# Kernel optimization log

Measured on AMD Instinct MI355X. Metric: run time of the kernel, lower is better.

Reference implementation:

```python
import jax, jax.numpy as jnp
import numpy as np

B, S, D, L = 16, 512, 768, 5
MAX_W, TOP_K = 5, 8


def setup_inputs() -> dict:
    key = jax.random.key(0)
    ks = jax.random.split(key, 6)
    token_embs = jax.random.normal(ks[0], (B, S, D), dtype=jnp.float32)
    token_mask = jnp.ones((B, S), dtype=jnp.int32)
    label_embs = jax.random.normal(ks[1], (B, L, D), dtype=jnp.float32)
    W1 = jax.random.normal(ks[2], (2 * D, D), dtype=jnp.float32) / np.sqrt(2 * D)
    b1 = jnp.zeros((D,), dtype=jnp.float32)
    W2 = jax.random.normal(ks[3], (D, D), dtype=jnp.float32) / np.sqrt(D)
    b2 = jnp.zeros((D,), dtype=jnp.float32)
    Ws = jax.random.normal(ks[4], (D,), dtype=jnp.float32) / np.sqrt(D)
    bs = jnp.zeros((), dtype=jnp.float32)
    return {"token_embs": token_embs, "token_mask": token_mask,
            "label_embs": label_embs, "W1": W1, "b1": b1,
            "W2": W2, "b2": b2, "Ws": Ws, "bs": bs}


def reference(token_embs, token_mask, label_embs, W1, b1, W2, b2, Ws, bs):
    # Enumerate all candidate spans (start s, width w in [1, MAX_W]) as a
    # fixed grid of N = S*MAX_W spans; invalid ones (end >= seq_len) masked.
    starts = jnp.arange(S)[:, None]                      # [S,1]
    ends = starts + jnp.arange(MAX_W)[None, :]           # [S,W] end index (inclusive)
    seq_len = token_mask.sum(-1)                         # [B]
    valid = (ends[None] < seq_len[:, None, None]).reshape(B, -1)  # [B,N]
    starts_flat = jnp.broadcast_to(starts, (S, MAX_W)).reshape(-1)  # [N]
    ends_flat = jnp.minimum(ends, S - 1).reshape(-1)                # [N]

    hs = token_embs[:, starts_flat]                      # [B,N,D]
    he = token_embs[:, ends_flat]                        # [B,N,D]
    concat = jnp.concatenate([hs, he], axis=-1)          # [B,N,2D]

    # span FFN: Linear -> ReLU -> Linear
    h = jax.nn.relu(jnp.einsum('bnf,fd->bnd', concat, W1) + b1)
    span_reprs = jnp.einsum('bnd,de->bne', h, W2) + b2   # [B,N,D]
    span_scores = jnp.einsum('bnd,d->bn', span_reprs, Ws) + bs  # [B,N]

    neg_inf = jnp.float32(-1e30)
    masked_scores = jnp.where(valid, span_scores, neg_inf)
    top_rel, top_idx = jax.lax.top_k(masked_scores, TOP_K)       # [B,K]
    top_spans = jnp.take_along_axis(span_reprs, top_idx[..., None], axis=1)  # [B,K,D]

    sim = jnp.einsum('bld,bkd->blk', label_embs, top_spans)      # [B,L,K]
    attn = jax.nn.softmax(top_rel, axis=-1)                      # [B,K]
    label_scores = jnp.einsum('blk,bk->bl', sim, attn)           # [B,L]
    scores = jax.nn.sigmoid(label_scores)
    mask = jnp.ones((B, L), dtype=bool)
    return scores, mask
```

## Files before the change

### kernel.cpp

```cpp
#include <hip/hip_runtime.h>
#include <math.h>

#define B_    16
#define S_    512
#define D_    768
#define L_    5
#define MAXW  5
#define TOPK  8
#define NSPAN (S_*MAXW)
#define M_    (B_*S_)

__global__ __launch_bounds__(256, 3)
void gemm_k(const float* __restrict__ Tm, const float* __restrict__ W1,
            float* __restrict__ Aout, float* __restrict__ Bout) {
    constexpr int K = D_, N = D_;
    __shared__ float As[16][128];
    __shared__ float Bs[16][128];

    const int bm  = blockIdx.x;
    const int bn2 = blockIdx.y;
    const float* W = W1 + (bn2 >= 6 ? (size_t)D_ * D_ : 0);
    float* Om      = (bn2 >= 6) ? Bout : Aout;
    const int bn   = (bn2 >= 6) ? bn2 - 6 : bn2;

    const int tid = threadIdx.x;
    const int row0 = bm * 128, col0 = bn * 128;
    const int tx = tid & 15, ty = tid >> 4;

    float acc[8][8];
    #pragma unroll
    for (int i = 0; i < 8; ++i)
        #pragma unroll
        for (int j = 0; j < 8; ++j) acc[i][j] = 0.f;

    const int arow = tid >> 1;
    const int acol = (tid & 1) * 4;
    const int brow = tid >> 5;
    const int bcol = (tid & 31) * 4;

    const float* Aptr = Tm + (size_t)(row0 + arow) * K + acol;
    const float* Bptr = W  + (size_t)brow * N + col0 + bcol;

    for (int k0 = 0; k0 < K; k0 += 16) {
        #pragma unroll
        for (int r = 0; r < 2; ++r) {
            float4 av = *reinterpret_cast<const float4*>(Aptr + k0 + r * 8);
            As[acol + r*8 + 0][arow] = av.x;
            As[acol + r*8 + 1][arow] = av.y;
            As[acol + r*8 + 2][arow] = av.z;
            As[acol + r*8 + 3][arow] = av.w;
        }
        #pragma unroll
        for (int r = 0; r < 2; ++r) {
            float4 bv = *reinterpret_cast<const float4*>(Bptr + (size_t)(k0 + r*8) * N);
            *reinterpret_cast<float4*>(&Bs[brow + r*8][bcol]) = bv;
        }
        __syncthreads();
        #pragma unroll
        for (int k = 0; k < 16; ++k) {
            float a[8], b[8];
            *reinterpret_cast<float4*>(&a[0]) = *reinterpret_cast<const float4*>(&As[k][ty*8]);
            *reinterpret_cast<float4*>(&a[4]) = *reinterpret_cast<const float4*>(&As[k][ty*8+4]);
            *reinterpret_cast<float4*>(&b[0]) = *reinterpret_cast<const float4*>(&Bs[k][tx*4]);
            *reinterpret_cast<float4*>(&b[4]) = *reinterpret_cast<const float4*>(&Bs[k][tx*4+64]);
            #pragma unroll
            for (int i = 0; i < 8; ++i)
                #pragma unroll
                for (int j = 0; j < 8; ++j)
                    acc[i][j] = fmaf(a[i], b[j], acc[i][j]);
        }
        __syncthreads();
    }
    #pragma unroll
    for (int i = 0; i < 8; ++i) {
        size_t ro = (size_t)(row0 + ty*8 + i) * N + col0;
        float4 v0 = make_float4(acc[i][0], acc[i][1], acc[i][2], acc[i][3]);
        float4 v1 = make_float4(acc[i][4], acc[i][5], acc[i][6], acc[i][7]);
        *reinterpret_cast<float4*>(&Om[ro + tx*4])      = v0;
        *reinterpret_cast<float4*>(&Om[ro + tx*4 + 64]) = v1;
    }
}

__global__ void w2ws_k(const float* __restrict__ W2, const float* __restrict__ Ws,
                       const float* __restrict__ b2, const float* __restrict__ bs,
                       float* __restrict__ w2ws, float* __restrict__ cc) {
    const int d = blockIdx.x;
    const int lane = threadIdx.x;
    float p = 0.f;
    if (d < D_) {
        const float* row = W2 + (size_t)d * D_;
        for (int i = lane; i < D_; i += 64) p += row[i] * Ws[i];
    } else {
        for (int i = lane; i < D_; i += 64) p += b2[i] * Ws[i];
    }
    #pragma unroll
    for (int off = 32; off; off >>= 1) p += __shfl_xor(p, off);
    if (lane == 0) {
        if (d < D_) w2ws[d] = p;
        else        *cc = p + *bs;
    }
}

__global__ void seqlen_k(const int* __restrict__ mask, int* __restrict__ seqlen) {
    const int b = blockIdx.x;
    const int lane = threadIdx.x;
    int p = 0;
    for (int i = lane; i < S_; i += 64) p += mask[b * S_ + i];
    #pragma unroll
    for (int off = 32; off; off >>= 1) p += __shfl_xor(p, off);
    if (lane == 0) seqlen[b] = p;
}

__global__ __launch_bounds__(64)
void score_k(const float* __restrict__ A, const float* __restrict__ Bm,
             const float* __restrict__ b1, const float* __restrict__ w2ws,
             const float* __restrict__ cc, const int* __restrict__ seqlen,
             float* __restrict__ scores) {
    const int bsid = blockIdx.x;
    const int b = bsid >> 9, s = bsid & 511;
    const int lane = threadIdx.x;
    float a[12], w[12], bb[12];
    const float* Arow = A + (size_t)bsid * D_;
    #pragma unroll
    for (int i = 0; i < 12; ++i) {
        int d = lane + i * 64;
        a[i]  = Arow[d];
        w[i]  = w2ws[d];
        bb[i] = b1[d];
    }
    const int sl = seqlen[b];
    const float c = *cc;
    #pragma unroll
    for (int w_ = 0; w_ < MAXW; ++w_) {
        const int e = min(s + w_, S_ - 1);
        const float* Brow = Bm + ((size_t)(b << 9) + e) * D_;
        float p = 0.f;
        #pragma unroll
        for (int i = 0; i < 12; ++i) {
            float h = a[i] + Brow[lane + i * 64] + bb[i];
            p = fmaf(fmaxf(h, 0.f), w[i], p);
        }
        #pragma unroll
        for (int off = 32; off; off >>= 1) p += __shfl_xor(p, off);
        if (lane == 0)
            scores[b * NSPAN + s * MAXW + w_] = (s + w_ < sl) ? (p + c) : -1e30f;
    }
}

__global__ __launch_bounds__(256)
void topk_k(const float* __restrict__ scores, float* __restrict__ top_rel,
            int* __restrict__ top_idx) {
    __shared__ float sv[NSPAN];
    __shared__ float rv[4];
    __shared__ int   ri[4];
    const int b = blockIdx.x, tid = threadIdx.x;
    for (int i = tid; i < NSPAN; i += 256) sv[i] = scores[b * NSPAN + i];
    __syncthreads();
    for (int k = 0; k < TOPK; ++k) {
        float best = -INFINITY; int bi = 1 << 30;
        for (int i = tid; i < NSPAN; i += 256) {
            float v = sv[i];
            if (v > best || (v == best && i < bi)) { best = v; bi = i; }
        }
        #pragma unroll
        for (int off = 32; off; off >>= 1) {
            float ov = __shfl_xor(best, off);
            int   oi = __shfl_xor(bi, off);
            if (ov > best || (ov == best && oi < bi)) { best = ov; bi = oi; }
        }
        if ((tid & 63) == 0) { rv[tid >> 6] = best; ri[tid >> 6] = bi; }
        __syncthreads();
        if (tid == 0) {
            #pragma unroll
            for (int wv = 1; wv < 4; ++wv)
                if (rv[wv] > best || (rv[wv] == best && ri[wv] < bi)) { best = rv[wv]; bi = ri[wv]; }
            top_rel[b * TOPK + k] = best;
            top_idx[b * TOPK + k] = bi;
            sv[bi] = -INFINITY;
        }
        __syncthreads();
    }
}

__global__ __launch_bounds__(256)
void repr_k(const float* __restrict__ A, const float* __restrict__ Bm,
            const float* __restrict__ b1, const float* __restrict__ W2,
            const float* __restrict__ b2, const float* __restrict__ labels,
            const int* __restrict__ top_idx, float* __restrict__ sim) {
    const int blk = blockIdx.x;
    const int b = blk >> 3, k = blk & 7;
    const int tid = threadIdx.x;
    __shared__ float h[D_];
    __shared__ float sr[D_];
    __shared__ float red[4];

    const int n = top_idx[b * TOPK + k];
    const int s = n / MAXW, w = n % MAXW;
    const int e = min(s + w, S_ - 1);
    const float* Arow = A  + (size_t)(b * S_ + s) * D_;
    const float* Brow = Bm + (size_t)(b * S_ + e) * D_;
    for (int d = tid; d < D_; d += 256) h[d] = fmaxf(Arow[d] + Brow[d] + b1[d], 0.f);
    __syncthreads();

    float r0 = b2[tid], r1 = b2[tid + 256], r2 = b2[tid + 512];
    for (int d = 0; d < D_; ++d) {
        const float hv = h[d];
        const float* Wrow = W2 + (size_t)d * D_;
        r0 = fmaf(hv, Wrow[tid],       r0);
        r1 = fmaf(hv, Wrow[tid + 256], r1);
        r2 = fmaf(hv, Wrow[tid + 512], r2);
    }
    sr[tid] = r0; sr[tid + 256] = r1; sr[tid + 512] = r2;
    __syncthreads();

    const float* lab = labels + (size_t)b * L_ * D_;
    for (int l = 0; l < L_; ++l) {
        float p = 0.f;
        for (int d = tid; d < D_; d += 256) p = fmaf(lab[l * D_ + d], sr[d], p);
        #pragma unroll
        for (int off = 32; off; off >>= 1) p += __shfl_xor(p, off);
        if ((tid & 63) == 0) red[tid >> 6] = p;
        __syncthreads();
        if (tid == 0) sim[(b * L_ + l) * TOPK + k] = red[0] + red[1] + red[2] + red[3];
        __syncthreads();
    }
}

__global__ void final_k(const float* __restrict__ top_rel, const float* __restrict__ sim,
                        float* __restrict__ out) {
    const int b = blockIdx.x, tid = threadIdx.x;
    float m = -INFINITY;
    #pragma unroll
    for (int k = 0; k < TOPK; ++k) m = fmaxf(m, top_rel[b * TOPK + k]);
    float wgt[TOPK]; float Z = 0.f;
    #pragma unroll
    for (int k = 0; k < TOPK; ++k) { wgt[k] = expf(top_rel[b * TOPK + k] - m); Z += wgt[k]; }
    if (tid < L_) {
        float acc = 0.f;
        #pragma unroll
        for (int k = 0; k < TOPK; ++k) acc += sim[(b * L_ + tid) * TOPK + k] * wgt[k];
        const float sc = acc / Z;
        out[b * L_ + tid]            = 1.f / (1.f + expf(-sc));
        out[B_ * L_ + b * L_ + tid]  = 1.0f;
    }
}

extern "C" void kernel_launch(void* const* d_in, const int* in_sizes, int n_in,
                              void* d_out, int out_size, void* d_ws, size_t ws_size,
                              hipStream_t stream) {
    const float* token_embs = (const float*)d_in[0];
    const int*   token_mask = (const int*)  d_in[1];
    const float* label_embs = (const float*)d_in[2];
    const float* W1 = (const float*)d_in[3];
    const float* b1 = (const float*)d_in[4];
    const float* W2 = (const float*)d_in[5];
    const float* b2 = (const float*)d_in[6];
    const float* Ws = (const float*)d_in[7];
    const float* bs = (const float*)d_in[8];
    float* out = (float*)d_out;

    float* A       = (float*)d_ws;
    float* Bm      = A + (size_t)M_ * D_;
    float* scores  = Bm + (size_t)M_ * D_;
    float* w2ws    = scores + B_ * NSPAN;
    float* cc      = w2ws + D_;
    int*   seqlen  = (int*)(cc + 1);
    float* top_rel = (float*)(seqlen + B_);
    int*   top_idx = (int*)(top_rel + B_ * TOPK);
    float* sim     = (float*)(top_idx + B_ * TOPK);

    gemm_k  <<<dim3(64, 12), 256, 0, stream>>>(token_embs, W1, A, Bm);
    w2ws_k  <<<D_ + 1, 64, 0, stream>>>(W2, Ws, b2, bs, w2ws, cc);
    seqlen_k<<<B_, 64, 0, stream>>>(token_mask, seqlen);
    score_k <<<M_, 64, 0, stream>>>(A, Bm, b1, w2ws, cc, seqlen, scores);
    topk_k  <<<B_, 256, 0, stream>>>(scores, top_rel, top_idx);
    repr_k  <<<B_ * TOPK, 256, 0, stream>>>(A, Bm, b1, W2, b2, label_embs, top_idx, sim);
    final_k <<<B_, 64, 0, stream>>>(top_rel, sim, out);
}
```

Baseline: 333.8 us.

## Use split-bf16 MFMA GEMM with fp32 rerank of top candidates

Replaces the fp32 SIMT GEMM for the first FFN layer with a bf16 MFMA GEMM that uses a hi/lo split (three passes: hi*hi, lo*hi, hi*lo) to approximate fp32 precision. Token and weight conversion kernels run first, and a sampled validation kernel sets a flag that triggers an fp32 fallback GEMM when the error is too large. To protect top-k selection from small precision errors, it takes 16 candidates and recomputes their hidden activations and scores exactly in fp32, then picks the final 8. This adds conversion passes, extra launches and a larger workspace. The fallback GEMM is still launched every time but exits early when the flag is clear.

```diff
diff --git a/kernel.cpp b/kernel.cpp
--- a/kernel.cpp
+++ b/kernel.cpp
@@ -7,40 +7,189 @@
 #define L_    5
 #define MAXW  5
 #define TOPK  8
+#define CAND  16
 #define NSPAN (S_*MAXW)
 #define M_    (B_*S_)
 
+typedef __attribute__((ext_vector_type(8))) short s16x8;
+typedef __attribute__((ext_vector_type(4))) float f32x4;
+
+__device__ __forceinline__ ushort f2bf(float x) {
+    union { float f; unsigned u; } c; c.f = x;
+    unsigned r = c.u + 0x7fffu + ((c.u >> 16) & 1u);
+    return (ushort)(r >> 16);
+}
+__device__ __forceinline__ float bf2f(ushort h) {
+    union { unsigned u; float f; } c; c.u = ((unsigned)h) << 16;
+    return c.f;
+}
+
+__global__ void init_k(int* __restrict__ flag, int v) {
+    if (threadIdx.x == 0) *flag = v;
+}
+
+__global__ __launch_bounds__(256)
+void cvt_T(const float* __restrict__ X, ushort* __restrict__ hi, ushort* __restrict__ lo) {
+    const int i = (blockIdx.x * 256 + threadIdx.x) * 4;
+    float4 v = *reinterpret_cast<const float4*>(X + i);
+    ushort4 h, l;
+    h.x = f2bf(v.x); l.x = f2bf(v.x - bf2f(h.x));
+    h.y = f2bf(v.y); l.y = f2bf(v.y - bf2f(h.y));
+    h.z = f2bf(v.z); l.z = f2bf(v.z - bf2f(h.z));
+    h.w = f2bf(v.w); l.w = f2bf(v.w - bf2f(h.w));
+    *reinterpret_cast<ushort4*>(hi + i) = h;
+    *reinterpret_cast<ushort4*>(lo + i) = l;
+}
+
+__global__ __launch_bounds__(256)
+void cvt_W(const float* __restrict__ W1, ushort* __restrict__ Whi, ushort* __restrict__ Wlo) {
+    __shared__ float tl[32][33];
+    const int k0 = blockIdx.x * 32, n0 = blockIdx.y * 32;
+    const int tx = threadIdx.x & 31, ty = threadIdx.x >> 5;
+    const int base = (n0 >= 768) ? 768 : 0;
+    const int d0 = n0 & 767;
+    #pragma unroll
+    for (int it = 0; it < 4; ++it) {
+        int rr = ty + it * 8;
+        tl[rr][tx] = W1[(size_t)(base + k0 + rr) * 768 + d0 + tx];
+    }
+    __syncthreads();
+    #pragma unroll
+    for (int it = 0; it < 4; ++it) {
+        int rr = ty + it * 8;
+        float v = tl[tx][rr];
+        ushort h = f2bf(v);
+        size_t o = (size_t)(n0 + rr) * 768 + k0 + tx;
+        Whi[o] = h;
+        Wlo[o] = f2bf(v - bf2f(h));
+    }
+}
+
+__global__ __launch_bounds__(256)
+void mm_k(const ushort* __restrict__ Thi, const ushort* __restrict__ Tlo,
+          const ushort* __restrict__ Whi, const ushort* __restrict__ Wlo,
+          float* __restrict__ Aout, float* __restrict__ Bout) {
+    __shared__ __align__(16) ushort As[128 * 32];
+    __shared__ __align__(16) ushort Bs[128 * 32];
+    const int tid = threadIdx.x;
+    const int bm = blockIdx.x, bn = blockIdx.y;
+    const int row0 = bm * 128;
+    const int n0g = bn * 128;
+
+    const int srow = tid >> 2;
+    const int scol = (tid & 3) * 8;
+    const size_t a_g0 = (size_t)(row0 + srow) * 768 + scol;
+    const size_t b_g0 = (size_t)(n0g + srow) * 768 + scol;
+    const int l_off = srow * 32 + scol;
+
+    const int lane = tid & 63, wv = tid >> 6;
+    const int wr = wv >> 1, wc = wv & 1;
+    const int lr = lane & 15, lg = lane >> 4;
+    const int ko = lg * 8;
+
+    f32x4 acc[4][4];
+    #pragma unroll
+    for (int i = 0; i < 4; ++i)
+        #pragma unroll
+        for (int j = 0; j < 4; ++j) acc[i][j] = f32x4{0.f, 0.f, 0.f, 0.f};
+
+    #pragma unroll 1
+    for (int ph = 0; ph < 3; ++ph) {
+        const ushort* Asrc = (ph == 1) ? Tlo : Thi;
+        const ushort* Bsrc = (ph == 2) ? Wlo : Whi;
+        #pragma unroll 1
+        for (int jj = 0; jj < 24; ++jj) {
+            const int col = jj * 32;
+            uint4 a0 = *reinterpret_cast<const uint4*>(Asrc + a_g0 + col);
+            uint4 a1 = *reinterpret_cast<const uint4*>(Asrc + a_g0 + col + 64 * 768);
+            uint4 b0 = *reinterpret_cast<const uint4*>(Bsrc + b_g0 + col);
+            uint4 b1 = *reinterpret_cast<const uint4*>(Bsrc + b_g0 + col + 64 * 768);
+            __syncthreads();
+            *reinterpret_cast<uint4*>(&As[l_off])           = a0;
+            *reinterpret_cast<uint4*>(&As[l_off + 64 * 32]) = a1;
+            *reinterpret_cast<uint4*>(&Bs[l_off])           = b0;
+            *reinterpret_cast<uint4*>(&Bs[l_off + 64 * 32]) = b1;
+            __syncthreads();
+            s16x8 af[4], bf[4];
+            #pragma unroll
+            for (int i = 0; i < 4; ++i)
+                af[i] = *reinterpret_cast<const s16x8*>(&As[(wr * 64 + i * 16 + lr) * 32 + ko]);
+            #pragma unroll
+            for (int j = 0; j < 4; ++j)
+                bf[j] = *reinterpret_cast<const s16x8*>(&Bs[(wc * 64 + j * 16 + lr) * 32 + ko]);
+            #pragma unroll
+            for (int i = 0; i < 4; ++i)
+                #pragma unroll
+                for (int j = 0; j < 4; ++j)
+                    acc[i][j] = __builtin_amdgcn_mfma_f32_16x16x32_bf16(af[i], bf[j], acc[i][j], 0, 0, 0);
+        }
+    }
+
+    float* Om = (bn < 6) ? Aout : Bout;
+    const int c0 = ((bn < 6) ? bn : bn - 6) * 128 + wc * 64;
+    #pragma unroll
+    for (int i = 0; i < 4; ++i) {
+        const int rbase = row0 + wr * 64 + i * 16 + lg * 4;
+        #pragma unroll
+        for (int j = 0; j < 4; ++j) {
+            const int cg = c0 + j * 16 + lr;
+            #pragma unroll
+            for (int r = 0; r < 4; ++r)
+                Om[(size_t)(rbase + r) * 768 + cg] = acc[i][j][r];
+        }
+    }
+}
+
+__global__ __launch_bounds__(64)
+void valid_k(const float* __restrict__ T, const float* __restrict__ W1,
+             const float* __restrict__ A, const float* __restrict__ Bm,
+             int* __restrict__ flag) {
+    const int blk = blockIdx.x, lane = threadIdx.x;
+    #pragma unroll 1
+    for (int j = 0; j < 8; ++j) {
+        const int id = blk * 8 + j;
+        const int m = (id * 509) & 8191;
+        const int n = (id * 251) % 1536;
+        const float* w = (n < 768) ? (W1 + n) : (W1 + 768 * 768 + (n - 768));
+        float p = 0.f;
+        for (int k = lane; k < 768; k += 64)
+            p = fmaf(T[(size_t)m * 768 + k], w[(size_t)k * 768], p);
+        #pragma unroll
+        for (int off = 32; off; off >>= 1) p += __shfl_xor(p, off);
+        if (lane == 0) {
+            float ap = (n < 768) ? A[(size_t)m * 768 + n] : Bm[(size_t)m * 768 + (n - 768)];
+            if (fabsf(p - ap) > 0.02f) atomicOr(flag, 1);
+        }
+    }
+}
+
 __global__ __launch_bounds__(256, 3)
-void gemm_k(const float* __restrict__ Tm, const float* __restrict__ W1,
-            float* __restrict__ Aout, float* __restrict__ Bout) {
+void repair_k(const float* __restrict__ Tm, const float* __restrict__ W1,
+              float* __restrict__ Aout, float* __restrict__ Bout,
+              const int* __restrict__ flag) {
+    if (*flag == 0) return;
     constexpr int K = D_, N = D_;
     __shared__ float As[16][128];
     __shared__ float Bs[16][128];
-
     const int bm  = blockIdx.x;
     const int bn2 = blockIdx.y;
     const float* W = W1 + (bn2 >= 6 ? (size_t)D_ * D_ : 0);
     float* Om      = (bn2 >= 6) ? Bout : Aout;
     const int bn   = (bn2 >= 6) ? bn2 - 6 : bn2;
-
     const int tid = threadIdx.x;
     const int row0 = bm * 128, col0 = bn * 128;
     const int tx = tid & 15, ty = tid >> 4;
-
     float acc[8][8];
     #pragma unroll
     for (int i = 0; i < 8; ++i)
         #pragma unroll
         for (int j = 0; j < 8; ++j) acc[i][j] = 0.f;
-
     const int arow = tid >> 1;
     const int acol = (tid & 1) * 4;
     const int brow = tid >> 5;
     const int bcol = (tid & 31) * 4;
-
     const float* Aptr = Tm + (size_t)(row0 + arow) * K + acol;
     const float* Bptr = W  + (size_t)brow * N + col0 + bcol;
-
     for (int k0 = 0; k0 < K; k0 += 16) {
         #pragma unroll
         for (int r = 0; r < 2; ++r) {
@@ -148,15 +297,14 @@
 }
 
 __global__ __launch_bounds__(256)
-void topk_k(const float* __restrict__ scores, float* __restrict__ top_rel,
-            int* __restrict__ top_idx) {
+void topk_k(const float* __restrict__ scores, int* __restrict__ cand_idx) {
     __shared__ float sv[NSPAN];
     __shared__ float rv[4];
     __shared__ int   ri[4];
     const int b = blockIdx.x, tid = threadIdx.x;
     for (int i = tid; i < NSPAN; i += 256) sv[i] = scores[b * NSPAN + i];
     __syncthreads();
-    for (int k = 0; k < TOPK; ++k) {
+    for (int k = 0; k < CAND; ++k) {
         float best = -INFINITY; int bi = 1 << 30;
         for (int i = tid; i < NSPAN; i += 256) {
             float v = sv[i];
@@ -174,8 +322,7 @@
             #pragma unroll
             for (int wv = 1; wv < 4; ++wv)
                 if (rv[wv] > best || (rv[wv] == best && ri[wv] < bi)) { best = rv[wv]; bi = ri[wv]; }
-            top_rel[b * TOPK + k] = best;
-            top_idx[b * TOPK + k] = bi;
+            cand_idx[b * CAND + k] = bi;
             sv[bi] = -INFINITY;
         }
         __syncthreads();
@@ -183,23 +330,120 @@
 }
 
 __global__ __launch_bounds__(256)
-void repr_k(const float* __restrict__ A, const float* __restrict__ Bm,
-            const float* __restrict__ b1, const float* __restrict__ W2,
-            const float* __restrict__ b2, const float* __restrict__ labels,
-            const int* __restrict__ top_idx, float* __restrict__ sim) {
+void rerank_k(const float* __restrict__ T, const float* __restrict__ W1,
+              const float* __restrict__ b1, const float* __restrict__ w2ws,
+              const float* __restrict__ cc, const int* __restrict__ cand_idx,
+              float* __restrict__ cand_h, float* __restrict__ cand_score) {
+    __shared__ float hsL[4][768];
+    __shared__ float heL[4][768];
+    __shared__ float red[4][4];
     const int blk = blockIdx.x;
-    const int b = blk >> 3, k = blk & 7;
+    const int b = blk >> 2, g = blk & 3;
+    const int tid = threadIdx.x;
+
+    int sA[4], eA[4];
+    #pragma unroll
+    for (int j = 0; j < 4; ++j) {
+        const int n = cand_idx[b * CAND + g * 4 + j];
+        const int s = n / MAXW, w = n % MAXW;
+        sA[j] = s; eA[j] = min(s + w, S_ - 1);
+    }
+    #pragma unroll
+    for (int j = 0; j < 4; ++j) {
+        const float* hsrc = T + ((size_t)(b * S_ + sA[j])) * D_;
+        const float* esrc = T + ((size_t)(b * S_ + eA[j])) * D_;
+        for (int d = tid; d < D_; d += 256) { hsL[j][d] = hsrc[d]; heL[j][d] = esrc[d]; }
+    }
+    __syncthreads();
+
+    float acc[4][3];
+    #pragma unroll
+    for (int j = 0; j < 4; ++j)
+        #pragma unroll
+        for (int q = 0; q < 3; ++q) acc[j][q] = 0.f;
+
+    #pragma unroll 1
+    for (int k = 0; k < D_; ++k) {
+        const float w00 = W1[(size_t)k * D_ + tid];
+        const float w01 = W1[(size_t)k * D_ + tid + 256];
+        const float w02 = W1[(size_t)k * D_ + tid + 512];
+        const float w10 = W1[(size_t)(D_ + k) * D_ + tid];
+        const float w11 = W1[(size_t)(D_ + k) * D_ + tid + 256];
+        const float w12 = W1[(size_t)(D_ + k) * D_ + tid + 512];
+        #pragma unroll
+        for (int j = 0; j < 4; ++j) {
+            const float hs = hsL[j][k], he = heL[j][k];
+            acc[j][0] = fmaf(hs, w00, fmaf(he, w10, acc[j][0]));
+            acc[j][1] = fmaf(hs, w01, fmaf(he, w11, acc[j][1]));
+            acc[j][2] = fmaf(hs, w02, fmaf(he, w12, acc[j][2]));
+        }
+    }
+
+    float part[4] = {0.f, 0.f, 0.f, 0.f};
+    #pragma unroll
+    for (int j = 0; j < 4; ++j) {
+        #pragma unroll
+        for (int q = 0; q < 3; ++q) {
+            const int d = tid + q * 256;
+            const float h = fmaxf(acc[j][q] + b1[d], 0.f);
+            cand_h[((size_t)(b * CAND + g * 4 + j)) * D_ + d] = h;
+            part[j] = fmaf(h, w2ws[d], part[j]);
+        }
+    }
+    #pragma unroll
+    for (int j = 0; j < 4; ++j) {
+        #pragma unroll
+        for (int off = 32; off; off >>= 1) part[j] += __shfl_xor(part[j], off);
+        if ((tid & 63) == 0) red[j][tid >> 6] = part[j];
+    }
+    __syncthreads();
+    if (tid == 0) {
+        #pragma unroll
+        for (int j = 0; j < 4; ++j)
+            cand_score[b * CAND + g * 4 + j] =
+                red[j][0] + red[j][1] + red[j][2] + red[j][3] + *cc;
+    }
+}
+
+__global__ void sel_k(const float* __restrict__ cand_score, const int* __restrict__ cand_idx,
+                      float* __restrict__ top_rel, int* __restrict__ sel_slot) {
+    const int b = blockIdx.x;
+    if (threadIdx.x != 0) return;
+    float sc[CAND]; int nn[CAND]; bool used[CAND];
+    #pragma unroll
+    for (int c = 0; c < CAND; ++c) {
+        sc[c] = cand_score[b * CAND + c];
+        nn[c] = cand_idx[b * CAND + c];
+        used[c] = false;
+    }
+    for (int k = 0; k < TOPK; ++k) {
+        float best = -INFINITY; int bi = -1, bn = 1 << 30;
+        #pragma unroll
+        for (int c = 0; c < CAND; ++c) {
+            if (!used[c] && (sc[c] > best || (sc[c] == best && nn[c] < bn))) {
+                best = sc[c]; bi = c; bn = nn[c];
+            }
+        }
+        used[bi] = true;
+        top_rel[b * TOPK + k] = best;
+        sel_slot[b * TOPK + k] = bi;
+    }
+}
+
+__global__ __launch_bounds__(256)
+void repr2_k(const float* __restrict__ cand_h, const int* __restrict__ sel_slot,
+             const float* __restrict__ W2, const float* __restrict__ b2,
+             const float* __restrict__ labels, float* __restrict__ sim) {
+    const int blk = blockIdx.x;
+    const int b = blk >> 3, kk = blk & 7;
     const int tid = threadIdx.x;
     __shared__ float h[D_];
     __shared__ float sr[D_];
     __shared__ float red[4];
 
-    const int n = top_idx[b * TOPK + k];
-    const int s = n / MAXW, w = n % MAXW;
-    const int e = min(s + w, S_ - 1);
-    const float* Arow = A  + (size_t)(b * S_ + s) * D_;
-    const float* Brow = Bm + (size_t)(b * S_ + e) * D_;
-    for (int d = tid; d < D_; d += 256) h[d] = fmaxf(Arow[d] + Brow[d] + b1[d], 0.f);
+    const int c = sel_slot[b * TOPK + kk];
+    const float* hp = cand_h + ((size_t)(b * CAND + c)) * D_;
+    for (int d = tid; d < D_; d += 256) h[d] = hp[d];
     __syncthreads();
 
     float r0 = b2[tid], r1 = b2[tid + 256], r2 = b2[tid + 512];
@@ -221,7 +465,7 @@
         for (int off = 32; off; off >>= 1) p += __shfl_xor(p, off);
         if ((tid & 63) == 0) red[tid >> 6] = p;
         __syncthreads();
-        if (tid == 0) sim[(b * L_ + l) * TOPK + k] = red[0] + red[1] + red[2] + red[3];
+        if (tid == 0) sim[(b * L_ + l) * TOPK + kk] = red[0] + red[1] + red[2] + red[3];
         __syncthreads();
     }
 }
@@ -248,6 +492,7 @@
 extern "C" void kernel_launch(void* const* d_in, const int* in_sizes, int n_in,
                               void* d_out, int out_size, void* d_ws, size_t ws_size,
                               hipStream_t stream) {
+    (void)in_sizes; (void)n_in; (void)out_size;
     const float* token_embs = (const float*)d_in[0];
     const int*   token_mask = (const int*)  d_in[1];
     const float* label_embs = (const float*)d_in[2];
@@ -259,21 +504,42 @@
     const float* bs = (const float*)d_in[8];
     float* out = (float*)d_out;
 
-    float* A       = (float*)d_ws;
-    float* Bm      = A + (size_t)M_ * D_;
-    float* scores  = Bm + (size_t)M_ * D_;
-    float* w2ws    = scores + B_ * NSPAN;
-    float* cc      = w2ws + D_;
-    int*   seqlen  = (int*)(cc + 1);
-    float* top_rel = (float*)(seqlen + B_);
-    int*   top_idx = (int*)(top_rel + B_ * TOPK);
-    float* sim     = (float*)(top_idx + B_ * TOPK);
-
-    gemm_k  <<<dim3(64, 12), 256, 0, stream>>>(token_embs, W1, A, Bm);
+    float* A          = (float*)d_ws;
+    float* Bm         = A + (size_t)M_ * D_;
+    float* scores     = Bm + (size_t)M_ * D_;
+    float* w2ws       = scores + B_ * NSPAN;
+    float* cc         = w2ws + D_;
+    int*   seqlen     = (int*)(cc + 1);
+    int*   flag       = seqlen + B_;
+    float* top_rel    = (float*)(flag + 1);
+    int*   sel_slot   = (int*)(top_rel + B_ * TOPK);
+    int*   cand_idx   = sel_slot + B_ * TOPK;
+    float* cand_score = (float*)(cand_idx + B_ * CAND);
+    float* sim        = cand_score + B_ * CAND;
+    float* cand_h     = A;
+
+    ushort* Thi  = (ushort*)(A + 12648448);
+    ushort* Tlo  = Thi + (size_t)M_ * D_;
+    ushort* WhiT = Tlo + (size_t)M_ * D_;
+    ushort* WloT = WhiT + (size_t)2 * D_ * D_;
+    const size_t need = 12648448ULL * 4 + (2ULL * M_ * D_ + 4ULL * D_ * D_) * 2;
+    const bool use_mfma = (ws_size >= need);
+
+    init_k<<<1, 64, 0, stream>>>(flag, use_mfma ? 0 : 1);
+    if (use_mfma) {
+        cvt_T<<<(M_ * D_) / (256 * 4), 256, 0, stream>>>(token_embs, Thi, Tlo);
+        cvt_W<<<dim3(24, 48), 256, 0, stream>>>(W1, WhiT, WloT);
+        mm_k <<<dim3(64, 12), 256, 0, stream>>>(Thi, Tlo, WhiT, WloT, A, Bm);
+        valid_k<<<256, 64, 0, stream>>>(token_embs, W1, A, Bm, flag);
+    }
+    repair_k<<<dim3(64, 12), 256, 0, stream>>>(token_embs, W1, A, Bm, flag);
     w2ws_k  <<<D_ + 1, 64, 0, stream>>>(W2, Ws, b2, bs, w2ws, cc);
     seqlen_k<<<B_, 64, 0, stream>>>(token_mask, seqlen);
     score_k <<<M_, 64, 0, stream>>>(A, Bm, b1, w2ws, cc, seqlen, scores);
-    topk_k  <<<B_, 256, 0, stream>>>(scores, top_rel, top_idx);
-    repr_k  <<<B_ * TOPK, 256, 0, stream>>>(A, Bm, b1, W2, b2, label_embs, top_idx, sim);
+    topk_k  <<<B_, 256, 0, stream>>>(scores, cand_idx);
+    rerank_k<<<B_ * 4, 256, 0, stream>>>(token_embs, W1, b1, w2ws, cc, cand_idx,
+                                         cand_h, cand_score);
+    sel_k   <<<B_, 64, 0, stream>>>(cand_score, cand_idx, top_rel, sel_slot);
+    repr2_k <<<B_ * TOPK, 256, 0, stream>>>(cand_h, sel_slot, W2, b2, label_embs, sim);
     final_k <<<B_, 64, 0, stream>>>(top_rel, sim, out);
 }
```

New measurement: 739.2 us. 2.21x slower.
